# Performance work log

Hardware: AMD Instinct MI355X
Metric: run time of the kernel (lower is better)

The kernel has to match this reference:

```python
import jax, jax.numpy as jnp
import numpy as np

IN_IM_SZ = 224   # network input size (in_im_sz)
OUT = 7          # RoIAlign output size (out_size)
SCALE = 1.0 / 16.0  # spatial scale feature/input


def _roi_align_one(feat, boxes):
    # feat: [C, Hf, Wf]; boxes: [P, 4] in network-input coords (x1,y1,x2,y2)
    C, H, W = feat.shape
    b = boxes * SCALE
    x1, y1, x2, y2 = b[:, 0], b[:, 1], b[:, 2], b[:, 3]
    bw = (x2 - x1) / OUT
    bh = (y2 - y1) / OUT
    off = jnp.arange(OUT, dtype=feat.dtype) + 0.5
    xs = x1[:, None] + off[None, :] * bw[:, None]   # [P, OUT]
    ys = y1[:, None] + off[None, :] * bh[:, None]   # [P, OUT]
    P = boxes.shape[0]
    X = jnp.broadcast_to(jnp.clip(xs[:, None, :], 0.0, W - 1), (P, OUT, OUT))
    Y = jnp.broadcast_to(jnp.clip(ys[:, :, None], 0.0, H - 1), (P, OUT, OUT))
    x0 = jnp.clip(jnp.floor(X).astype(jnp.int32), 0, W - 1)
    y0 = jnp.clip(jnp.floor(Y).astype(jnp.int32), 0, H - 1)
    x1i = jnp.minimum(x0 + 1, W - 1)
    y1i = jnp.minimum(y0 + 1, H - 1)
    lx = X - x0
    ly = Y - y0
    # gathers: [C, P, OUT, OUT]
    f00 = feat[:, y0, x0]
    f01 = feat[:, y0, x1i]
    f10 = feat[:, y1i, x0]
    f11 = feat[:, y1i, x1i]
    val = (f00 * (1 - ly) * (1 - lx) + f01 * (1 - ly) * lx
           + f10 * ly * (1 - lx) + f11 * ly * lx)
    return jnp.transpose(val, (1, 0, 2, 3))  # [P, C, OUT, OUT]


_roi_align = jax.vmap(_roi_align_one)  # [B,C,H,W],[B,P,4] -> [B,P,C,OUT,OUT]


def setup_inputs() -> dict:
    key = jax.random.key(0)
    ks = jax.random.split(key, 12)
    B, NH, NO, C, HF = 4, 16, 16, 1024, 14
    im_h, im_w = 480, 640
    features = jax.random.normal(ks[0], (B, C, HF, HF), jnp.float32)

    def make_boxes(k1, k2, k3, k4, k5, n, cls):
        x1 = jax.random.uniform(k1, (B, n)) * (im_w * 0.5)
        y1 = jax.random.uniform(k2, (B, n)) * (im_h * 0.5)
        w = 20.0 + jax.random.uniform(k3, (B, n)) * (im_w * 0.4)
        h = 20.0 + jax.random.uniform(k4, (B, n)) * (im_h * 0.4)
        x2 = jnp.minimum(x1 + w, im_w - 1.0)
        y2 = jnp.minimum(y1 + h, im_h - 1.0)
        score = jax.random.uniform(k5, (B, n))
        return jnp.stack([x1, y1, x2, y2, score, cls], axis=-1).astype(jnp.float32)

    H_Box = make_boxes(ks[1], ks[2], ks[3], ks[4], ks[5], NH,
                       jnp.ones((B, NH)))  # class 1 = person
    o_cls = jax.random.randint(ks[11], (B, NO), 1, 19).astype(jnp.float32)
    O_Box = make_boxes(ks[6], ks[7], ks[8], ks[9], ks[10], NO, o_cls)
    return {"features": features, "H_Box": H_Box, "O_Box": O_Box,
            "im_h": im_h, "im_w": im_w}


def reference(features, H_Box, O_Box, im_h, im_w):
    B, NH = H_Box.shape[:2]
    NO = O_Box.shape[1]
    C = features.shape[1]
    rW = IN_IM_SZ / float(im_w)
    rH = IN_IM_SZ / float(im_h)
    sc = jnp.array([rW, rH, rW, rH], features.dtype)

    # per-box RoIAlign (human / object nodes)
    H_Node = _roi_align(features, H_Box[..., :4] * sc)  # [B,NH,C,7,7]
    O_Node = _roi_align(features, O_Box[..., :4] * sc)  # [B,NO,C,7,7]

    # pairwise union boxes (image coords), as in H_O_BBOX
    h4 = H_Box[:, :, None, :4]  # [B,NH,1,4]
    o4 = O_Box[:, None, :, :4]  # [B,1,NO,4]
    ux1 = jnp.minimum(o4[..., 0], h4[..., 0])
    uy1 = jnp.minimum(o4[..., 1], h4[..., 1])
    ux2 = jnp.maximum(o4[..., 2], h4[..., 2])
    uy2 = jnp.maximum(o4[..., 3], h4[..., 3])
    U = jnp.stack([ux1, uy1, ux2, uy2], axis=-1)  # [B,NH,NO,4]
    H_O_Node = _roi_align(features, (U * sc).reshape(B, NH * NO, 4))
    H_O_Node = H_O_Node.reshape(B, NH, NO, C, OUT, OUT)

    # geometry encoding (box_encode), vectorized over all pairs
    hx1, hy1, hx2, hy2 = [h4[..., i] for i in range(4)]  # [B,NH,1]
    ox1, oy1, ox2, oy2 = [o4[..., i] for i in range(4)]  # [B,1,NO]
    h_cx, h_cy = (hx1 + hx2) / 2, (hy1 + hy2) / 2
    h_w, h_h = hx2 - hx1, hy2 - hy1
    o_cx, o_cy = (ox1 + ox2) / 2, (oy1 + oy2) / 2
    o_w, o_h = ox2 - ox1, oy2 - oy1
    dxc = h_cx - o_cx
    dyc = h_cy - o_cy
    d_x = jnp.abs(dxc) / h_w * 100.0
    d_y = jnp.abs(dyc) / h_h * 100.0
    d_xy = jnp.sqrt(dxc ** 2 + dyc ** 2) / (h_w + h_h) * 100.0
    dx_ratio = jnp.abs(dxc) / im_w * 100.0
    dy_ratio = jnp.abs(dyc) / im_h * 100.0
    det_y = jnp.where(jnp.abs(dyc) > 1e-5, dyc,
                      jnp.where(dyc > 0, 1e-5, -1e-5))
    angle = jnp.arctan(dxc / det_y)
    area_scale = (o_w * o_h) / (h_w * h_h)
    o_scale = o_h / o_w
    ix1 = jnp.maximum(hx1, ox1)
    iy1 = jnp.maximum(hy1, oy1)
    ix2 = jnp.minimum(hx2, ox2)
    iy2 = jnp.minimum(hy2, oy2)
    inter = jnp.maximum(ix2 - ix1, 0.0) * jnp.maximum(iy2 - iy1, 0.0)
    union = h_w * h_h + o_w * o_h - inter
    iou = jnp.where(inter > 0, inter / union, 0.0)
    geometry = jnp.stack(
        [jnp.broadcast_to(t, (B, NH, NO)) for t in
         (d_x, d_y, d_xy, dx_ratio, dy_ratio, angle, area_scale, o_scale, iou)],
        axis=-1)  # [B,NH,NO,9]

    # area_sacale_ratio for H, O and union boxes
    im_area = float(im_h) * float(im_w)
    h_ratio = (H_Box[..., 2] - H_Box[..., 0]) * (H_Box[..., 3] - H_Box[..., 1]) / im_area * 100.0
    o_ratio = (O_Box[..., 2] - O_Box[..., 0]) * (O_Box[..., 3] - O_Box[..., 1]) / im_area * 100.0
    ho_ratio = (ux2 - ux1) * (uy2 - uy1) / im_area * 100.0

    return (H_Node, O_Node, H_O_Node, geometry, h_ratio, o_ratio, ho_ratio)
```

## Files before the change

### kernel.cpp

```cpp
#include <hip/hip_runtime.h>


#define C_CH   1024
#define HW     14
#define PLANE  196
#define OUTS   7
#define TILE   (C_CH * OUTS * OUTS)
#define OFF_O  3211264
#define OFF_U  6422528
#define OFF_G  57802752
#define OFF_HR 57811968
#define OFF_OR 57812032
#define OFF_UR 57812096

#define CH_PER_BLK   32
#define ROI_PER_BLK  16
#define CH_PER_WAVE  8

#define SCR    (CH_PER_BLK * PLANE)
#define WSCR   (CH_PER_WAVE * 49)
#define BXS    (SCR + 4 * WSCR)

__global__ __launch_bounds__(256) void roi_align_kernel(
    const float* __restrict__ feat,
    const float* __restrict__ HBox,
    const float* __restrict__ OBox,
    const int* __restrict__ im_h_p,
    const int* __restrict__ im_w_p,
    float* __restrict__ out)
{
    __shared__ float lds[BXS + 192];

    const int c0 = blockIdx.x * CH_PER_BLK;
    const int g0 = blockIdx.y * ROI_PER_BLK;
    const int b  = g0 / 288;

    {
        const float4* g4 = (const float4*)(feat + ((size_t)b * C_CH + c0) * PLANE);
        float4* l4 = (float4*)lds;
        for (int i = threadIdx.x; i < (CH_PER_BLK * PLANE / 4); i += 256)
            l4[i] = g4[i];
    }
    if (threadIdx.x < 96)
        lds[BXS + threadIdx.x] = HBox[b * 96 + threadIdx.x];
    else if (threadIdx.x < 192)
        lds[BXS + threadIdx.x] = OBox[b * 96 + (threadIdx.x - 96)];
    __syncthreads();

    const int lane = threadIdx.x & 63;
    const int wave = threadIdx.x >> 6;
    if (lane >= 49) return;

    const int pos = lane;
    const int oy = pos / 7;
    const int ox = pos - oy * 7;

    const float im_w = (float)(*im_w_p);
    const float im_h = (float)(*im_h_p);
    const float scx = (224.0f / im_w) * (1.0f / 16.0f);
    const float scy = (224.0f / im_h) * (1.0f / 16.0f);

    const float* ldw = lds + (wave * CH_PER_WAVE) * PLANE;
    const int cw = c0 + wave * CH_PER_WAVE;

    float* sw = lds + SCR + wave * WSCR;
    const float4* sv = (const float4*)sw;
    const float* hbx = lds + BXS;
    const float* obx = lds + BXS + 96;

    for (int ri = 0; ri < ROI_PER_BLK; ++ri) {
        const int g = g0 + ri;
        const int j = g - b * 288;

        float x1, y1, x2, y2;
        size_t outBase;
        if (j < 16) {
            const float* bx = hbx + j * 6;
            x1 = bx[0]; y1 = bx[1]; x2 = bx[2]; y2 = bx[3];
            outBase = (size_t)(b * 16 + j) * TILE;
        } else if (j < 32) {
            const float* bx = obx + (j - 16) * 6;
            x1 = bx[0]; y1 = bx[1]; x2 = bx[2]; y2 = bx[3];
            outBase = OFF_O + (size_t)(b * 16 + (j - 16)) * TILE;
        } else {
            const int u = j - 32;
            const float* hb = hbx + (u >> 4) * 6;
            const float* ob = obx + (u & 15) * 6;
            x1 = fminf(ob[0], hb[0]);
            y1 = fminf(ob[1], hb[1]);
            x2 = fmaxf(ob[2], hb[2]);
            y2 = fmaxf(ob[3], hb[3]);
            outBase = OFF_U + (size_t)(b * 256 + u) * TILE;
        }

        const float bx1 = x1 * scx;
        const float by1 = y1 * scy;
        const float bw = (x2 * scx - bx1) * (1.0f / OUTS);
        const float bh = (y2 * scy - by1) * (1.0f / OUTS);
        float X = bx1 + ((float)ox + 0.5f) * bw;
        float Y = by1 + ((float)oy + 0.5f) * bh;
        X = fminf(fmaxf(X, 0.0f), (float)(HW - 1));
        Y = fminf(fmaxf(Y, 0.0f), (float)(HW - 1));
        const int x0 = min((int)floorf(X), HW - 2);
        const int y0 = min((int)floorf(Y), HW - 2);
        const float lx = X - (float)x0;
        const float ly = Y - (float)y0;
        const float w00 = (1.0f - ly) * (1.0f - lx);
        const float w01 = (1.0f - ly) * lx;
        const float w10 = ly * (1.0f - lx);
        const float w11 = ly * lx;
        const int off = y0 * HW + x0;

        const float* lp = ldw + off;
#pragma unroll
        for (int k = 0; k < CH_PER_WAVE; ++k) {
            const float f00 = lp[0];
            const float f01 = lp[1];
            const float f10 = lp[HW];
            const float f11 = lp[HW + 1];
            sw[k * 49 + pos] = f00 * w00 + f01 * w01 + f10 * w10 + f11 * w11;
            lp += PLANE;
        }

        asm volatile("s_waitcnt lgkmcnt(0)" ::: "memory");

        float4* og = (float4*)(out + outBase + (size_t)cw * 49);
        const float4 a = sv[pos];
        const float4 c = sv[pos + 49];
        og[pos] = a;
        og[pos + 49] = c;
    }
}

__global__ __launch_bounds__(256) void geom_kernel(
    const float* __restrict__ HBox,
    const float* __restrict__ OBox,
    const int* __restrict__ im_h_p,
    const int* __restrict__ im_w_p,
    float* __restrict__ geo,
    float* __restrict__ h_ratio,
    float* __restrict__ o_ratio,
    float* __restrict__ ho_ratio)
{
    const int p = blockIdx.x * 256 + threadIdx.x;
    if (p >= 1024) return;
    const float im_w = (float)(*im_w_p);
    const float im_h = (float)(*im_h_p);
    const float im_area = im_h * im_w;

    const int b = p >> 8;
    const int h = (p >> 4) & 15;
    const int o = p & 15;
    const float* hb = HBox + (b * 16 + h) * 6;
    const float* ob = OBox + (b * 16 + o) * 6;
    const float hx1 = hb[0], hy1 = hb[1], hx2 = hb[2], hy2 = hb[3];
    const float ox1 = ob[0], oy1 = ob[1], ox2 = ob[2], oy2 = ob[3];

    const float h_cx = (hx1 + hx2) * 0.5f, h_cy = (hy1 + hy2) * 0.5f;
    const float h_w = hx2 - hx1, h_h = hy2 - hy1;
    const float o_cx = (ox1 + ox2) * 0.5f, o_cy = (oy1 + oy2) * 0.5f;
    const float o_w = ox2 - ox1, o_h = oy2 - oy1;

    const float dxc = h_cx - o_cx;
    const float dyc = h_cy - o_cy;
    const float adx = fabsf(dxc), ady = fabsf(dyc);

    const float d_x = adx / h_w * 100.0f;
    const float d_y = ady / h_h * 100.0f;
    const float d_xy = sqrtf(dxc * dxc + dyc * dyc) / (h_w + h_h) * 100.0f;
    const float dx_ratio = adx / im_w * 100.0f;
    const float dy_ratio = ady / im_h * 100.0f;
    const float det_y = (ady > 1e-5f) ? dyc : ((dyc > 0.0f) ? 1e-5f : -1e-5f);
    const float angle = atanf(dxc / det_y);
    const float area_scale = (o_w * o_h) / (h_w * h_h);
    const float o_scale = o_h / o_w;

    const float ix1 = fmaxf(hx1, ox1), iy1 = fmaxf(hy1, oy1);
    const float ix2 = fminf(hx2, ox2), iy2 = fminf(hy2, oy2);
    const float inter = fmaxf(ix2 - ix1, 0.0f) * fmaxf(iy2 - iy1, 0.0f);
    const float uni = h_w * h_h + o_w * o_h - inter;
    const float iou = (inter > 0.0f) ? inter / uni : 0.0f;

    float* g = geo + (size_t)p * 9;
    g[0] = d_x; g[1] = d_y; g[2] = d_xy;
    g[3] = dx_ratio; g[4] = dy_ratio; g[5] = angle;
    g[6] = area_scale; g[7] = o_scale; g[8] = iou;

    const float ux1 = fminf(ox1, hx1), uy1 = fminf(oy1, hy1);
    const float ux2 = fmaxf(ox2, hx2), uy2 = fmaxf(oy2, hy2);
    ho_ratio[p] = (ux2 - ux1) * (uy2 - uy1) / im_area * 100.0f;

    if (p < 64) {
        const float* hb2 = HBox + p * 6;
        h_ratio[p] = (hb2[2] - hb2[0]) * (hb2[3] - hb2[1]) / im_area * 100.0f;
        const float* ob2 = OBox + p * 6;
        o_ratio[p] = (ob2[2] - ob2[0]) * (ob2[3] - ob2[1]) / im_area * 100.0f;
    }
}

extern "C" void kernel_launch(void* const* d_in, const int* in_sizes, int n_in,
                              void* d_out, int out_size, void* d_ws, size_t ws_size,
                              hipStream_t stream) {
    const float* feat = (const float*)d_in[0];
    const float* HBox = (const float*)d_in[1];
    const float* OBox = (const float*)d_in[2];
    const int* im_h = (const int*)d_in[3];
    const int* im_w = (const int*)d_in[4];
    float* out = (float*)d_out;

    dim3 grid(32, 72);
    roi_align_kernel<<<grid, 256, 0, stream>>>(feat, HBox, OBox, im_h, im_w, out);

    geom_kernel<<<4, 256, 0, stream>>>(HBox, OBox, im_h, im_w,
                                       out + OFF_G, out + OFF_HR,
                                       out + OFF_OR, out + OFF_UR);
}
```

Measured before the change: 244.4 us.

## Fuse geometry into RoIAlign kernel, halve channels per block, write outputs directly

Moves the geometry computation into extra blocks (blockIdx.y==72) of the RoIAlign kernel, which removes the second kernel launch. It halves the channels per block to 16 (4 per wave), doubles the grid in x, and sets a launch-bounds occupancy hint. The LDS staging plus float4 store path is replaced by direct scalar global stores, 49 floats per channel per wave. This raises occupancy and cuts LDS use, but each feature plane is reloaded by more blocks and the output stores are narrower.

```diff
diff --git a/kernel.cpp b/kernel.cpp
--- a/kernel.cpp
+++ b/kernel.cpp
@@ -13,15 +13,13 @@
 #define OFF_OR 57812032
 #define OFF_UR 57812096
 
-#define CH_PER_BLK   32
+#define CH_PER_BLK   16
 #define ROI_PER_BLK  16
-#define CH_PER_WAVE  8
+#define CH_PER_WAVE  4
 
-#define SCR    (CH_PER_BLK * PLANE)
-#define WSCR   (CH_PER_WAVE * 49)
-#define BXS    (SCR + 4 * WSCR)
+#define BXS    (CH_PER_BLK * PLANE)
 
-__global__ __launch_bounds__(256) void roi_align_kernel(
+__global__ __launch_bounds__(256, 8) void roi_align_kernel(
     const float* __restrict__ feat,
     const float* __restrict__ HBox,
     const float* __restrict__ OBox,
@@ -30,6 +28,65 @@
     float* __restrict__ out)
 {
     __shared__ float lds[BXS + 192];
+
+    const float im_w = (float)(*im_w_p);
+    const float im_h = (float)(*im_h_p);
+
+    if (blockIdx.y == 72) {
+        if (blockIdx.x >= 4) return;
+        const int p = blockIdx.x * 256 + threadIdx.x;
+        const float im_area = im_h * im_w;
+
+        const int b = p >> 8;
+        const int h = (p >> 4) & 15;
+        const int o = p & 15;
+        const float* hb = HBox + (b * 16 + h) * 6;
+        const float* ob = OBox + (b * 16 + o) * 6;
+        const float hx1 = hb[0], hy1 = hb[1], hx2 = hb[2], hy2 = hb[3];
+        const float ox1 = ob[0], oy1 = ob[1], ox2 = ob[2], oy2 = ob[3];
+
+        const float h_cx = (hx1 + hx2) * 0.5f, h_cy = (hy1 + hy2) * 0.5f;
+        const float h_w = hx2 - hx1, h_h = hy2 - hy1;
+        const float o_cx = (ox1 + ox2) * 0.5f, o_cy = (oy1 + oy2) * 0.5f;
+        const float o_w = ox2 - ox1, o_h = oy2 - oy1;
+
+        const float dxc = h_cx - o_cx;
+        const float dyc = h_cy - o_cy;
+        const float adx = fabsf(dxc), ady = fabsf(dyc);
+
+        const float d_x = adx / h_w * 100.0f;
+        const float d_y = ady / h_h * 100.0f;
+        const float d_xy = sqrtf(dxc * dxc + dyc * dyc) / (h_w + h_h) * 100.0f;
+        const float dx_ratio = adx / im_w * 100.0f;
+        const float dy_ratio = ady / im_h * 100.0f;
+        const float det_y = (ady > 1e-5f) ? dyc : ((dyc > 0.0f) ? 1e-5f : -1e-5f);
+        const float angle = atanf(dxc / det_y);
+        const float area_scale = (o_w * o_h) / (h_w * h_h);
+        const float o_scale = o_h / o_w;
+
+        const float ix1 = fmaxf(hx1, ox1), iy1 = fmaxf(hy1, oy1);
+        const float ix2 = fminf(hx2, ox2), iy2 = fminf(hy2, oy2);
+        const float inter = fmaxf(ix2 - ix1, 0.0f) * fmaxf(iy2 - iy1, 0.0f);
+        const float uni = h_w * h_h + o_w * o_h - inter;
+        const float iou = (inter > 0.0f) ? inter / uni : 0.0f;
+
+        float* g = out + OFF_G + (size_t)p * 9;
+        g[0] = d_x; g[1] = d_y; g[2] = d_xy;
+        g[3] = dx_ratio; g[4] = dy_ratio; g[5] = angle;
+        g[6] = area_scale; g[7] = o_scale; g[8] = iou;
+
+        const float ux1 = fminf(ox1, hx1), uy1 = fminf(oy1, hy1);
+        const float ux2 = fmaxf(ox2, hx2), uy2 = fmaxf(oy2, hy2);
+        out[OFF_UR + p] = (ux2 - ux1) * (uy2 - uy1) / im_area * 100.0f;
+
+        if (p < 64) {
+            const float* hb2 = HBox + p * 6;
+            out[OFF_HR + p] = (hb2[2] - hb2[0]) * (hb2[3] - hb2[1]) / im_area * 100.0f;
+            const float* ob2 = OBox + p * 6;
+            out[OFF_OR + p] = (ob2[2] - ob2[0]) * (ob2[3] - ob2[1]) / im_area * 100.0f;
+        }
+        return;
+    }
 
     const int c0 = blockIdx.x * CH_PER_BLK;
     const int g0 = blockIdx.y * ROI_PER_BLK;
@@ -55,16 +112,12 @@
     const int oy = pos / 7;
     const int ox = pos - oy * 7;
 
-    const float im_w = (float)(*im_w_p);
-    const float im_h = (float)(*im_h_p);
     const float scx = (224.0f / im_w) * (1.0f / 16.0f);
     const float scy = (224.0f / im_h) * (1.0f / 16.0f);
 
     const float* ldw = lds + (wave * CH_PER_WAVE) * PLANE;
     const int cw = c0 + wave * CH_PER_WAVE;
 
-    float* sw = lds + SCR + wave * WSCR;
-    const float4* sv = (const float4*)sw;
     const float* hbx = lds + BXS;
     const float* obx = lds + BXS + 96;
 
@@ -112,89 +165,16 @@
         const int off = y0 * HW + x0;
 
         const float* lp = ldw + off;
+        float* op = out + outBase + (size_t)cw * 49 + pos;
 #pragma unroll
         for (int k = 0; k < CH_PER_WAVE; ++k) {
             const float f00 = lp[0];
             const float f01 = lp[1];
             const float f10 = lp[HW];
             const float f11 = lp[HW + 1];
-            sw[k * 49 + pos] = f00 * w00 + f01 * w01 + f10 * w10 + f11 * w11;
+            op[49 * k] = f00 * w00 + f01 * w01 + f10 * w10 + f11 * w11;
             lp += PLANE;
         }
-
-        asm volatile("s_waitcnt lgkmcnt(0)" ::: "memory");
-
-        float4* og = (float4*)(out + outBase + (size_t)cw * 49);
-        const float4 a = sv[pos];
-        const float4 c = sv[pos + 49];
-        og[pos] = a;
-        og[pos + 49] = c;
-    }
-}
-
-__global__ __launch_bounds__(256) void geom_kernel(
-    const float* __restrict__ HBox,
-    const float* __restrict__ OBox,
-    const int* __restrict__ im_h_p,
-    const int* __restrict__ im_w_p,
-    float* __restrict__ geo,
-    float* __restrict__ h_ratio,
-    float* __restrict__ o_ratio,
-    float* __restrict__ ho_ratio)
-{
-    const int p = blockIdx.x * 256 + threadIdx.x;
-    if (p >= 1024) return;
-    const float im_w = (float)(*im_w_p);
-    const float im_h = (float)(*im_h_p);
-    const float im_area = im_h * im_w;
-
-    const int b = p >> 8;
-    const int h = (p >> 4) & 15;
-    const int o = p & 15;
-    const float* hb = HBox + (b * 16 + h) * 6;
-    const float* ob = OBox + (b * 16 + o) * 6;
-    const float hx1 = hb[0], hy1 = hb[1], hx2 = hb[2], hy2 = hb[3];
-    const float ox1 = ob[0], oy1 = ob[1], ox2 = ob[2], oy2 = ob[3];
-
-    const float h_cx = (hx1 + hx2) * 0.5f, h_cy = (hy1 + hy2) * 0.5f;
-    const float h_w = hx2 - hx1, h_h = hy2 - hy1;
-    const float o_cx = (ox1 + ox2) * 0.5f, o_cy = (oy1 + oy2) * 0.5f;
-    const float o_w = ox2 - ox1, o_h = oy2 - oy1;
-
-    const float dxc = h_cx - o_cx;
-    const float dyc = h_cy - o_cy;
-    const float adx = fabsf(dxc), ady = fabsf(dyc);
-
-    const float d_x = adx / h_w * 100.0f;
-    const float d_y = ady / h_h * 100.0f;
-    const float d_xy = sqrtf(dxc * dxc + dyc * dyc) / (h_w + h_h) * 100.0f;
-    const float dx_ratio = adx / im_w * 100.0f;
-    const float dy_ratio = ady / im_h * 100.0f;
-    const float det_y = (ady > 1e-5f) ? dyc : ((dyc > 0.0f) ? 1e-5f : -1e-5f);
-    const float angle = atanf(dxc / det_y);
-    const float area_scale = (o_w * o_h) / (h_w * h_h);
-    const float o_scale = o_h / o_w;
-
-    const float ix1 = fmaxf(hx1, ox1), iy1 = fmaxf(hy1, oy1);
-    const float ix2 = fminf(hx2, ox2), iy2 = fminf(hy2, oy2);
-    const float inter = fmaxf(ix2 - ix1, 0.0f) * fmaxf(iy2 - iy1, 0.0f);
-    const float uni = h_w * h_h + o_w * o_h - inter;
-    const float iou = (inter > 0.0f) ? inter / uni : 0.0f;
-
-    float* g = geo + (size_t)p * 9;
-    g[0] = d_x; g[1] = d_y; g[2] = d_xy;
-    g[3] = dx_ratio; g[4] = dy_ratio; g[5] = angle;
-    g[6] = area_scale; g[7] = o_scale; g[8] = iou;
-
-    const float ux1 = fminf(ox1, hx1), uy1 = fminf(oy1, hy1);
-    const float ux2 = fmaxf(ox2, hx2), uy2 = fmaxf(oy2, hy2);
-    ho_ratio[p] = (ux2 - ux1) * (uy2 - uy1) / im_area * 100.0f;
-
-    if (p < 64) {
-        const float* hb2 = HBox + p * 6;
-        h_ratio[p] = (hb2[2] - hb2[0]) * (hb2[3] - hb2[1]) / im_area * 100.0f;
-        const float* ob2 = OBox + p * 6;
-        o_ratio[p] = (ob2[2] - ob2[0]) * (ob2[3] - ob2[1]) / im_area * 100.0f;
     }
 }
 
@@ -208,10 +188,6 @@
     const int* im_w = (const int*)d_in[4];
     float* out = (float*)d_out;
 
-    dim3 grid(32, 72);
+    dim3 grid(64, 73);
     roi_align_kernel<<<grid, 256, 0, stream>>>(feat, HBox, OBox, im_h, im_w, out);
-
-    geom_kernel<<<4, 256, 0, stream>>>(HBox, OBox, im_h, im_w,
-                                       out + OFF_G, out + OFF_HR,
-                                       out + OFF_OR, out + OFF_UR);
 }
```

Measured after the change: 239.9 us (median of 2 runs). About the same (-1.9%).
